# Performance work log

Hardware: AMD Instinct MI355X
Metric: run time of the kernel (lower is better)

## Reference

```python
import jax, jax.numpy as jnp
import numpy as np

HIDDEN = 1024
NUM_HEADS = 16
GROUP_SIZE = 2
GROUP_NUM = NUM_HEADS // GROUP_SIZE
HEAD_DIM = HIDDEN // NUM_HEADS


def setup_inputs() -> dict:
    key = jax.random.key(0)
    ks = jax.random.split(key, 9)
    B, S = 1, 4096
    s = 0.02
    return {
        "hidden_state": jax.random.normal(ks[0], (B, S, HIDDEN), jnp.float32),
        "Wq": jax.random.normal(ks[1], (HIDDEN, HIDDEN), jnp.float32) * s,
        "bq": jnp.zeros((HIDDEN,), jnp.float32),
        "Wk": jax.random.normal(ks[2], (HIDDEN, GROUP_NUM * HEAD_DIM), jnp.float32) * s,
        "bk": jnp.zeros((GROUP_NUM * HEAD_DIM,), jnp.float32),
        "Wv": jax.random.normal(ks[3], (HIDDEN, GROUP_NUM * HEAD_DIM), jnp.float32) * s,
        "bv": jnp.zeros((GROUP_NUM * HEAD_DIM,), jnp.float32),
        "Wo": jax.random.normal(ks[4], (HIDDEN, HIDDEN), jnp.float32) * s,
        "bo": jnp.zeros((HIDDEN,), jnp.float32),
    }


def reference(hidden_state, Wq, bq, Wk, bk, Wv, bv, Wo, bo):
    B, S, _ = hidden_state.shape
    # projections
    q = hidden_state @ Wq + bq                      # [B,S,H*hd]
    k = hidden_state @ Wk + bk                      # [B,S,G*hd]
    v = hidden_state @ Wv + bv                      # [B,S,G*hd]
    q = q.reshape(B, S, NUM_HEADS, HEAD_DIM).transpose(0, 2, 1, 3)   # [B,H,S,hd]
    k = k.reshape(B, S, GROUP_NUM, HEAD_DIM).transpose(0, 2, 1, 3)   # [B,G,S,hd]
    v = v.reshape(B, S, GROUP_NUM, HEAD_DIM).transpose(0, 2, 1, 3)
    # expand KV heads: each kv head repeated group_size times consecutively
    k = jnp.repeat(k, GROUP_SIZE, axis=1)           # [B,H,S,hd]
    v = jnp.repeat(v, GROUP_SIZE, axis=1)
    scale = 1.0 / np.sqrt(HEAD_DIM).astype(np.float32)
    scores = jnp.einsum('bhqd,bhkd->bhqk', q, k) * scale   # [B,H,S,S]
    attn = jax.nn.softmax(scores, axis=-1)
    ctx = jnp.einsum('bhqk,bhkd->bhqd', attn, v)    # [B,H,S,hd]
    ctx = ctx.transpose(0, 2, 1, 3).reshape(B, S, HIDDEN)
    return ctx @ Wo + bo
```

## Files before the change

### kernel.cpp

```cpp
#include <hip/hip_runtime.h>
#include <hip/hip_bf16.h>
#include <cstdint>
#include <cstddef>

typedef __bf16 bf16x8 __attribute__((ext_vector_type(8)));
typedef float f32x4 __attribute__((ext_vector_type(4)));
typedef float f32x16 __attribute__((ext_vector_type(16)));
typedef uint32_t u32x4 __attribute__((ext_vector_type(4)));
typedef __hip_bfloat16 bf16h;

__device__ __forceinline__ unsigned short bf16bits(float f) {
  bf16h h = __float2bfloat16(f);
  return __builtin_bit_cast(unsigned short, h);
}
__device__ __forceinline__ float bf16tof(unsigned short u) {
  union { uint32_t i; float f; } v; v.i = (uint32_t)u << 16; return v.f;
}

__global__ void cast_f32_bf16(const float* __restrict__ src, bf16h* __restrict__ dst, int n) {
  int i = (blockIdx.x * blockDim.x + threadIdx.x) * 4;
  if (i >= n) return;
  float4 v = *reinterpret_cast<const float4*>(src + i);
  ushort4 o;
  o.x = bf16bits(v.x); o.y = bf16bits(v.y); o.z = bf16bits(v.z); o.w = bf16bits(v.w);
  *reinterpret_cast<ushort4*>(dst + i) = o;
}

__global__ void transpose_cast_f32(const float* __restrict__ src, bf16h* __restrict__ dst,
                                   int R, int C, float scale) {
  __shared__ float tile[32][33];
  int c0 = blockIdx.x * 32, r0 = blockIdx.y * 32;
  int tx = threadIdx.x, ty = threadIdx.y;
  #pragma unroll
  for (int i = 0; i < 32; i += 8)
    tile[ty + i][tx] = src[(size_t)(r0 + ty + i) * C + c0 + tx];
  __syncthreads();
  #pragma unroll
  for (int i = 0; i < 32; i += 8)
    dst[(size_t)(c0 + ty + i) * R + r0 + tx] = __float2bfloat16(tile[tx][ty + i] * scale);
}

__global__ void concat_bias(const float* __restrict__ bq, const float* __restrict__ bk,
                            const float* __restrict__ bv, float* __restrict__ bcat, float qscale) {
  int i = blockIdx.x * blockDim.x + threadIdx.x;
  if (i >= 2048) return;
  bcat[i] = (i < 1024) ? bq[i] * qscale : (i < 1536 ? bk[i - 1024] : bv[i - 1536]);
}

__device__ __forceinline__ void store_out(float* p, float v) { *p = v; }
__device__ __forceinline__ void store_out(bf16h* p, float v) { *p = __float2bfloat16(v); }

template <typename OutT>
__global__ __launch_bounds__(256) void gemm_bt(const bf16h* __restrict__ A, const bf16h* __restrict__ BT,
                                               const float* __restrict__ bias, OutT* __restrict__ C,
                                               int ldc, bf16h* __restrict__ vtg, int vcol0,
                                               int M, int N, int K) {
  __shared__ __align__(16) bf16h As[128 * 64];
  __shared__ __align__(16) bf16h Bs[128 * 64];
  const int tid = threadIdx.x;
  const int lane = tid & 63;
  const int m0 = blockIdx.y * 128, n0 = blockIdx.x * 128;
  const int wid = tid >> 6, wr = wid >> 1, wc = wid & 1;
  const int cl = lane & 15, rg = lane >> 4;
  const int srow = tid >> 3, scol = (tid & 7) * 8;
  f32x4 acc[4][4] = {};

  for (int k0 = 0; k0 < K; k0 += 64) {
    __syncthreads();
    #pragma unroll
    for (int i = 0; i < 4; ++i) {
      int r = i * 32 + srow;
      __builtin_amdgcn_global_load_lds(
          (__attribute__((address_space(1))) void*)(A + (size_t)(m0 + r) * K + k0 + scol),
          (__attribute__((address_space(3))) void*)(As + i * 2048 + tid * 8), 16, 0, 0);
    }
    #pragma unroll
    for (int i = 0; i < 4; ++i) {
      int r = i * 32 + srow;
      __builtin_amdgcn_global_load_lds(
          (__attribute__((address_space(1))) void*)(BT + (size_t)(n0 + r) * K + k0 + scol),
          (__attribute__((address_space(3))) void*)(Bs + i * 2048 + tid * 8), 16, 0, 0);
    }
    __syncthreads();
    #pragma unroll
    for (int ks = 0; ks < 2; ++ks) {
      bf16x8 af[4], bfr[4];
      #pragma unroll
      for (int mi = 0; mi < 4; ++mi)
        af[mi] = *reinterpret_cast<const bf16x8*>(As + (wr * 64 + mi * 16 + cl) * 64 + ks * 32 + rg * 8);
      #pragma unroll
      for (int ni = 0; ni < 4; ++ni)
        bfr[ni] = *reinterpret_cast<const bf16x8*>(Bs + (wc * 64 + ni * 16 + cl) * 64 + ks * 32 + rg * 8);
      #pragma unroll
      for (int mi = 0; mi < 4; ++mi)
        #pragma unroll
        for (int ni = 0; ni < 4; ++ni)
          acc[mi][ni] = __builtin_amdgcn_mfma_f32_16x16x32_bf16(af[mi], bfr[ni], acc[mi][ni], 0, 0, 0);
    }
  }
  if (n0 >= vcol0) {
    #pragma unroll
    for (int ni = 0; ni < 4; ++ni) {
      int col = n0 + wc * 64 + ni * 16 + cl;
      float bv = bias[col];
      #pragma unroll
      for (int mi = 0; mi < 4; ++mi) {
        int row0 = m0 + wr * 64 + mi * 16 + rg * 4;
        ushort4 o;
        o.x = bf16bits(acc[mi][ni][0] + bv);
        o.y = bf16bits(acc[mi][ni][1] + bv);
        o.z = bf16bits(acc[mi][ni][2] + bv);
        o.w = bf16bits(acc[mi][ni][3] + bv);
        *reinterpret_cast<ushort4*>(vtg + (size_t)(col - vcol0) * 4096 + row0) = o;
      }
    }
  } else {
    #pragma unroll
    for (int ni = 0; ni < 4; ++ni) {
      int col = n0 + wc * 64 + ni * 16 + cl;
      float bv = bias[col];
      #pragma unroll
      for (int mi = 0; mi < 4; ++mi) {
        #pragma unroll
        for (int j = 0; j < 4; ++j) {
          int row = m0 + wr * 64 + mi * 16 + rg * 4 + j;
          store_out(&C[(size_t)row * ldc + col], acc[mi][ni][j] + bv);
        }
      }
    }
  }
}

__global__ __launch_bounds__(256, 2) void attn_fwd(const bf16h* __restrict__ qk,
                                                   const bf16h* __restrict__ vt,
                                                   bf16h* __restrict__ part,
                                                   float* __restrict__ lpart) {
  __shared__ __align__(16) char smem[32768];
  const int tid = threadIdx.x, lane = tid & 63, wid = tid >> 6;
  const int l31 = lane & 31, hi = lane >> 5;
  const int h = blockIdx.y, g = h >> 1, c = blockIdx.z;
  const int q0 = blockIdx.x * 256 + wid * 64;
  const int kbase = c * 2048;

  bf16x8 qfA[4], qfB[4];
  {
    const bf16h* qrowA = qk + (size_t)(q0 + l31) * 1536 + h * 64 + hi * 8;
    const bf16h* qrowB = qrowA + (size_t)32 * 1536;
    #pragma unroll
    for (int ds = 0; ds < 4; ++ds) {
      qfA[ds] = *reinterpret_cast<const bf16x8*>(qrowA + ds * 16);
      qfB[ds] = *reinterpret_cast<const bf16x8*>(qrowB + ds * 16);
    }
  }

  f32x16 oA0, oA1, oB0, oB1;
  #pragma unroll
  for (int i = 0; i < 16; ++i) { oA0[i] = 0.f; oA1[i] = 0.f; oB0[i] = 0.f; oB1[i] = 0.f; }
  float lsumA = 0.f, lsumB = 0.f;

  auto stage = [&](int kk, int b) {
    char* kb = smem + b * 16384;
    char* vb = kb + 8192;
    #pragma unroll
    for (int i = 0; i < 2; ++i) {
      int slot = tid + i * 256;
      int r = slot >> 3, s = slot & 7, sx = s ^ (r & 7);
      __builtin_amdgcn_global_load_lds(
          (__attribute__((address_space(1))) void*)(qk + (size_t)(kk + r) * 1536 + 1024 + g * 64 + sx * 8),
          (__attribute__((address_space(3))) void*)(kb + slot * 16), 16, 0, 0);
      __builtin_amdgcn_global_load_lds(
          (__attribute__((address_space(1))) void*)(vt + (size_t)(g * 64 + r) * 4096 + kk + sx * 8),
          (__attribute__((address_space(3))) void*)(vb + slot * 16), 16, 0, 0);
    }
  };

  stage(kbase, 0);
  __syncthreads();
  int cur = 0;

  auto build_pa = [&](const f32x16& S, int u) -> bf16x8 {
    uint32_t w0, w1, w2, w3;
    asm("v_cvt_pk_bf16_f32 %0, %1, %2" : "=v"(w0) : "v"(S[8 * u + 0]), "v"(S[8 * u + 1]));
    asm("v_cvt_pk_bf16_f32 %0, %1, %2" : "=v"(w1) : "v"(S[8 * u + 2]), "v"(S[8 * u + 3]));
    asm("v_cvt_pk_bf16_f32 %0, %1, %2" : "=v"(w2) : "v"(S[8 * u + 4]), "v"(S[8 * u + 5]));
    asm("v_cvt_pk_bf16_f32 %0, %1, %2" : "=v"(w3) : "v"(S[8 * u + 6]), "v"(S[8 * u + 7]));
    asm("v_permlane32_swap_b32 %0, %1" : "+v"(w0), "+v"(w2));
    asm("v_permlane32_swap_b32 %0, %1" : "+v"(w1), "+v"(w3));
    u32x4 pw; pw[0] = w0; pw[1] = w1; pw[2] = w2; pw[3] = w3;
    return __builtin_bit_cast(bf16x8, pw);
  };

  for (int tt = 0; tt < 32; ++tt) {
    if (tt < 31) stage(kbase + (tt + 1) * 64, cur ^ 1);
    const char* kb = smem + cur * 16384;
    const char* vb = kb + 8192;

    f32x16 sA0, sA1, sB0, sB1;
    #pragma unroll
    for (int i = 0; i < 16; ++i) { sA0[i] = 0.f; sA1[i] = 0.f; sB0[i] = 0.f; sB1[i] = 0.f; }
    __builtin_amdgcn_s_setprio(1);
    #pragma unroll
    for (int ds = 0; ds < 4; ++ds) {
      int cb = 32 * ds + 16 * hi;
      int r0 = l31, r1 = 32 + l31;
      bf16x8 k0 = *reinterpret_cast<const bf16x8*>(kb + ((r0 * 128 + cb) ^ ((r0 & 7) << 4)));
      bf16x8 k1 = *reinterpret_cast<const bf16x8*>(kb + ((r1 * 128 + cb) ^ ((r1 & 7) << 4)));
      sA0 = __builtin_amdgcn_mfma_f32_32x32x16_bf16(k0, qfA[ds], sA0, 0, 0, 0);
      sA1 = __builtin_amdgcn_mfma_f32_32x32x16_bf16(k1, qfA[ds], sA1, 0, 0, 0);
      sB0 = __builtin_amdgcn_mfma_f32_32x32x16_bf16(k0, qfB[ds], sB0, 0, 0, 0);
      sB1 = __builtin_amdgcn_mfma_f32_32x32x16_bf16(k1, qfB[ds], sB1, 0, 0, 0);
    }
    __builtin_amdgcn_s_setprio(0);

    float rsA = 0.f, rsB = 0.f;
    #pragma unroll
    for (int r = 0; r < 16; ++r) {
      sA0[r] = __builtin_amdgcn_exp2f(sA0[r]); rsA += sA0[r];
      sA1[r] = __builtin_amdgcn_exp2f(sA1[r]); rsA += sA1[r];
      sB0[r] = __builtin_amdgcn_exp2f(sB0[r]); rsB += sB0[r];
      sB1[r] = __builtin_amdgcn_exp2f(sB1[r]); rsB += sB1[r];
    }
    lsumA += rsA + __shfl_xor(rsA, 32);
    lsumB += rsB + __shfl_xor(rsB, 32);

    __builtin_amdgcn_s_setprio(1);
    #pragma unroll
    for (int ks = 0; ks < 4; ++ks) {
      const int u = ks & 1;
      bf16x8 paA = build_pa(ks < 2 ? sA0 : sA1, u);
      bf16x8 paB = build_pa(ks < 2 ? sB0 : sB1, u);
      int cb = 32 * ks + 16 * hi;
      int r0 = l31, r1 = 32 + l31;
      bf16x8 vf0 = *reinterpret_cast<const bf16x8*>(vb + ((r0 * 128 + cb) ^ ((r0 & 7) << 4)));
      bf16x8 vf1 = *reinterpret_cast<const bf16x8*>(vb + ((r1 * 128 + cb) ^ ((r1 & 7) << 4)));
      oA0 = __builtin_amdgcn_mfma_f32_32x32x16_bf16(vf0, paA, oA0, 0, 0, 0);
      oA1 = __builtin_amdgcn_mfma_f32_32x32x16_bf16(vf1, paA, oA1, 0, 0, 0);
      oB0 = __builtin_amdgcn_mfma_f32_32x32x16_bf16(vf0, paB, oB0, 0, 0, 0);
      oB1 = __builtin_amdgcn_mfma_f32_32x32x16_bf16(vf1, paB, oB1, 0, 0, 0);
    }
    __builtin_amdgcn_s_setprio(0);

    __syncthreads();
    cur ^= 1;
  }

  {
    int qA = q0 + l31, qB = qA + 32;
    bf16h* pA = part + ((size_t)(c * 4096 + qA) * 16 + h) * 64;
    bf16h* pB = part + ((size_t)(c * 4096 + qB) * 16 + h) * 64;
    #pragma unroll
    for (int dh = 0; dh < 2; ++dh) {
      const f32x16& aA = dh ? oA1 : oA0;
      const f32x16& aB = dh ? oB1 : oB0;
      #pragma unroll
      for (int t = 0; t < 4; ++t) {
        int d0 = dh * 32 + 8 * t + 4 * hi;
        ushort4 sa, sb;
        sa.x = bf16bits(aA[4 * t + 0]); sa.y = bf16bits(aA[4 * t + 1]);
        sa.z = bf16bits(aA[4 * t + 2]); sa.w = bf16bits(aA[4 * t + 3]);
        sb.x = bf16bits(aB[4 * t + 0]); sb.y = bf16bits(aB[4 * t + 1]);
        sb.z = bf16bits(aB[4 * t + 2]); sb.w = bf16bits(aB[4 * t + 3]);
        *reinterpret_cast<ushort4*>(pA + d0) = sa;
        *reinterpret_cast<ushort4*>(pB + d0) = sb;
      }
    }
    if (hi == 0) {
      lpart[(size_t)(c * 4096 + qA) * 16 + h] = lsumA;
      lpart[(size_t)(c * 4096 + qB) * 16 + h] = lsumB;
    }
  }
}

__global__ __launch_bounds__(256) void combine_part(const bf16h* __restrict__ part,
                                                    const float* __restrict__ lpart,
                                                    bf16h* __restrict__ ctx) {
  int idx = blockIdx.x * 256 + threadIdx.x;
  int q = idx >> 4, h = idx & 15;
  const bf16h* p0 = part + ((size_t)q * 16 + h) * 64;
  const bf16h* p1 = p0 + (size_t)4096 * 1024;
  float inv = 1.0f / (lpart[(size_t)q * 16 + h] + lpart[(size_t)4096 * 16 + q * 16 + h]);
  bf16h* o = ctx + (size_t)q * 1024 + h * 64;
  #pragma unroll
  for (int w = 0; w < 8; ++w) {
    ushort4 a = *reinterpret_cast<const ushort4*>(p0 + w * 8);
    ushort4 b = *reinterpret_cast<const ushort4*>(p1 + w * 8);
    ushort4 c2 = *reinterpret_cast<const ushort4*>(p0 + w * 8 + 4);
    ushort4 d2 = *reinterpret_cast<const ushort4*>(p1 + w * 8 + 4);
    ushort4 r0, r1;
    r0.x = bf16bits((bf16tof(a.x) + bf16tof(b.x)) * inv);
    r0.y = bf16bits((bf16tof(a.y) + bf16tof(b.y)) * inv);
    r0.z = bf16bits((bf16tof(a.z) + bf16tof(b.z)) * inv);
    r0.w = bf16bits((bf16tof(a.w) + bf16tof(b.w)) * inv);
    r1.x = bf16bits((bf16tof(c2.x) + bf16tof(d2.x)) * inv);
    r1.y = bf16bits((bf16tof(c2.y) + bf16tof(d2.y)) * inv);
    r1.z = bf16bits((bf16tof(c2.z) + bf16tof(d2.z)) * inv);
    r1.w = bf16bits((bf16tof(c2.w) + bf16tof(d2.w)) * inv);
    *reinterpret_cast<ushort4*>(o + w * 8) = r0;
    *reinterpret_cast<ushort4*>(o + w * 8 + 4) = r1;
  }
}

extern "C" void kernel_launch(void* const* d_in, const int* in_sizes, int n_in,
                              void* d_out, int out_size, void* d_ws, size_t ws_size,
                              hipStream_t stream) {
  const float* hs = (const float*)d_in[0];
  const float* Wq = (const float*)d_in[1];
  const float* bq = (const float*)d_in[2];
  const float* Wk = (const float*)d_in[3];
  const float* bk = (const float*)d_in[4];
  const float* Wv = (const float*)d_in[5];
  const float* bv = (const float*)d_in[6];
  const float* Wo = (const float*)d_in[7];
  const float* bo = (const float*)d_in[8];
  float* out = (float*)d_out;

  const float QSCALE = 0.125f * 1.44269504088896f;

  char* ws = (char*)d_ws;
  const size_t MB = 1u << 20;
  bf16h* hb    = (bf16h*)(ws);
  bf16h* WcT   = (bf16h*)(ws + 8 * MB);
  bf16h* part  = (bf16h*)(ws);
  float* lpart = (float*)(ws + 16 * MB);
  bf16h* qk    = (bf16h*)(ws + 17 * MB);
  bf16h* ctx   = (bf16h*)(ws + 17 * MB);
  bf16h* vtg   = (bf16h*)(ws + 29 * MB);
  bf16h* WoT   = (bf16h*)(ws + 33 * MB);
  float* bcat  = (float*)(ws + 35 * MB);

  cast_f32_bf16<<<dim3(4096), dim3(256), 0, stream>>>(hs, hb, 4096 * 1024);
  transpose_cast_f32<<<dim3(32, 32), dim3(32, 8), 0, stream>>>(Wq, WcT, 1024, 1024, QSCALE);
  transpose_cast_f32<<<dim3(16, 32), dim3(32, 8), 0, stream>>>(Wk, WcT + 1024 * 1024, 1024, 512, 1.0f);
  transpose_cast_f32<<<dim3(16, 32), dim3(32, 8), 0, stream>>>(Wv, WcT + 1536 * 1024, 1024, 512, 1.0f);
  transpose_cast_f32<<<dim3(32, 32), dim3(32, 8), 0, stream>>>(Wo, WoT, 1024, 1024, 1.0f);
  concat_bias<<<dim3(8), dim3(256), 0, stream>>>(bq, bk, bv, bcat, QSCALE);
  gemm_bt<bf16h><<<dim3(16, 32), dim3(256), 0, stream>>>(hb, WcT, bcat, qk, 1536, vtg, 1536,
                                                         4096, 2048, 1024);
  attn_fwd<<<dim3(16, 16, 2), dim3(256), 0, stream>>>(qk, vtg, part, lpart);
  combine_part<<<dim3(256), dim3(256), 0, stream>>>(part, lpart, ctx);
  gemm_bt<float><<<dim3(8, 32), dim3(256), 0, stream>>>(ctx, WoT, bo, out, 1024, (bf16h*)nullptr,
                                                        0x40000000, 4096, 1024, 1024);
}
```

Before: 158.5 us.

## Load K/V fragments directly from global memory, dropping LDS staging and barriers

The attention kernel no longer stages K and V tiles into shared memory with double-buffered global_load_lds and per-iteration __syncthreads. Each wave now reads its K and V MFMA fragments straight from global memory, relying on L2/L1 caching to serve the reuse across the four waves of a block. The V loads are issued early so they overlap the exp2 pass, and the row-sum reduction is split into several independent accumulators to shorten its dependency chain. This removes barrier stalls and LDS traffic but loses the explicit prefetch, so every wave redundantly fetches the same K/V data and global load latency sits directly in the loop.

```diff
diff --git a/kernel.cpp b/kernel.cpp
--- a/kernel.cpp
+++ b/kernel.cpp
@@ -135,7 +135,6 @@
                                                    const bf16h* __restrict__ vt,
                                                    bf16h* __restrict__ part,
                                                    float* __restrict__ lpart) {
-  __shared__ __align__(16) char smem[32768];
   const int tid = threadIdx.x, lane = tid & 63, wid = tid >> 6;
   const int l31 = lane & 31, hi = lane >> 5;
   const int h = blockIdx.y, g = h >> 1, c = blockIdx.z;
@@ -153,30 +152,13 @@
     }
   }
 
+  const bf16h* kp = qk + (size_t)(kbase + l31) * 1536 + 1024 + g * 64 + 8 * hi;
+  const bf16h* vp = vt + (size_t)(g * 64 + l31) * 4096 + kbase + 8 * hi;
+
   f32x16 oA0, oA1, oB0, oB1;
   #pragma unroll
   for (int i = 0; i < 16; ++i) { oA0[i] = 0.f; oA1[i] = 0.f; oB0[i] = 0.f; oB1[i] = 0.f; }
   float lsumA = 0.f, lsumB = 0.f;
-
-  auto stage = [&](int kk, int b) {
-    char* kb = smem + b * 16384;
-    char* vb = kb + 8192;
-    #pragma unroll
-    for (int i = 0; i < 2; ++i) {
-      int slot = tid + i * 256;
-      int r = slot >> 3, s = slot & 7, sx = s ^ (r & 7);
-      __builtin_amdgcn_global_load_lds(
-          (__attribute__((address_space(1))) void*)(qk + (size_t)(kk + r) * 1536 + 1024 + g * 64 + sx * 8),
-          (__attribute__((address_space(3))) void*)(kb + slot * 16), 16, 0, 0);
-      __builtin_amdgcn_global_load_lds(
-          (__attribute__((address_space(1))) void*)(vt + (size_t)(g * 64 + r) * 4096 + kk + sx * 8),
-          (__attribute__((address_space(3))) void*)(vb + slot * 16), 16, 0, 0);
-    }
-  };
-
-  stage(kbase, 0);
-  __syncthreads();
-  int cur = 0;
 
   auto build_pa = [&](const f32x16& S, int u) -> bf16x8 {
     uint32_t w0, w1, w2, w3;
@@ -191,9 +173,8 @@
   };
 
   for (int tt = 0; tt < 32; ++tt) {
-    if (tt < 31) stage(kbase + (tt + 1) * 64, cur ^ 1);
-    const char* kb = smem + cur * 16384;
-    const char* vb = kb + 8192;
+    const bf16h* kt = kp + (size_t)(tt * 64) * 1536;
+    const bf16h* vtp = vp + tt * 64;
 
     f32x16 sA0, sA1, sB0, sB1;
     #pragma unroll
@@ -201,10 +182,8 @@
     __builtin_amdgcn_s_setprio(1);
     #pragma unroll
     for (int ds = 0; ds < 4; ++ds) {
-      int cb = 32 * ds + 16 * hi;
-      int r0 = l31, r1 = 32 + l31;
-      bf16x8 k0 = *reinterpret_cast<const bf16x8*>(kb + ((r0 * 128 + cb) ^ ((r0 & 7) << 4)));
-      bf16x8 k1 = *reinterpret_cast<const bf16x8*>(kb + ((r1 * 128 + cb) ^ ((r1 & 7) << 4)));
+      bf16x8 k0 = *reinterpret_cast<const bf16x8*>(kt + 16 * ds);
+      bf16x8 k1 = *reinterpret_cast<const bf16x8*>(kt + (size_t)32 * 1536 + 16 * ds);
       sA0 = __builtin_amdgcn_mfma_f32_32x32x16_bf16(k0, qfA[ds], sA0, 0, 0, 0);
       sA1 = __builtin_amdgcn_mfma_f32_32x32x16_bf16(k1, qfA[ds], sA1, 0, 0, 0);
       sB0 = __builtin_amdgcn_mfma_f32_32x32x16_bf16(k0, qfB[ds], sB0, 0, 0, 0);
@@ -212,14 +191,31 @@
     }
     __builtin_amdgcn_s_setprio(0);
 
-    float rsA = 0.f, rsB = 0.f;
-    #pragma unroll
-    for (int r = 0; r < 16; ++r) {
-      sA0[r] = __builtin_amdgcn_exp2f(sA0[r]); rsA += sA0[r];
-      sA1[r] = __builtin_amdgcn_exp2f(sA1[r]); rsA += sA1[r];
-      sB0[r] = __builtin_amdgcn_exp2f(sB0[r]); rsB += sB0[r];
-      sB1[r] = __builtin_amdgcn_exp2f(sB1[r]); rsB += sB1[r];
-    }
+    bf16x8 vf[4][2];
+    #pragma unroll
+    for (int ks = 0; ks < 4; ++ks) {
+      vf[ks][0] = *reinterpret_cast<const bf16x8*>(vtp + 16 * ks);
+      vf[ks][1] = *reinterpret_cast<const bf16x8*>(vtp + (size_t)32 * 4096 + 16 * ks);
+    }
+
+    float ra0 = 0.f, ra1 = 0.f, ra2 = 0.f, ra3 = 0.f;
+    float rb0 = 0.f, rb1 = 0.f, rb2 = 0.f, rb3 = 0.f;
+    #pragma unroll
+    for (int r = 0; r < 16; r += 4) {
+      #pragma unroll
+      for (int j = 0; j < 4; ++j) {
+        sA0[r + j] = __builtin_amdgcn_exp2f(sA0[r + j]);
+        sA1[r + j] = __builtin_amdgcn_exp2f(sA1[r + j]);
+        sB0[r + j] = __builtin_amdgcn_exp2f(sB0[r + j]);
+        sB1[r + j] = __builtin_amdgcn_exp2f(sB1[r + j]);
+      }
+      ra0 += sA0[r] + sA0[r + 1]; ra1 += sA0[r + 2] + sA0[r + 3];
+      ra2 += sA1[r] + sA1[r + 1]; ra3 += sA1[r + 2] + sA1[r + 3];
+      rb0 += sB0[r] + sB0[r + 1]; rb1 += sB0[r + 2] + sB0[r + 3];
+      rb2 += sB1[r] + sB1[r + 1]; rb3 += sB1[r + 2] + sB1[r + 3];
+    }
+    float rsA = (ra0 + ra1) + (ra2 + ra3);
+    float rsB = (rb0 + rb1) + (rb2 + rb3);
     lsumA += rsA + __shfl_xor(rsA, 32);
     lsumB += rsB + __shfl_xor(rsB, 32);
 
@@ -229,19 +225,12 @@
       const int u = ks & 1;
       bf16x8 paA = build_pa(ks < 2 ? sA0 : sA1, u);
       bf16x8 paB = build_pa(ks < 2 ? sB0 : sB1, u);
-      int cb = 32 * ks + 16 * hi;
-      int r0 = l31, r1 = 32 + l31;
-      bf16x8 vf0 = *reinterpret_cast<const bf16x8*>(vb + ((r0 * 128 + cb) ^ ((r0 & 7) << 4)));
-      bf16x8 vf1 = *reinterpret_cast<const bf16x8*>(vb + ((r1 * 128 + cb) ^ ((r1 & 7) << 4)));
-      oA0 = __builtin_amdgcn_mfma_f32_32x32x16_bf16(vf0, paA, oA0, 0, 0, 0);
-      oA1 = __builtin_amdgcn_mfma_f32_32x32x16_bf16(vf1, paA, oA1, 0, 0, 0);
-      oB0 = __builtin_amdgcn_mfma_f32_32x32x16_bf16(vf0, paB, oB0, 0, 0, 0);
-      oB1 = __builtin_amdgcn_mfma_f32_32x32x16_bf16(vf1, paB, oB1, 0, 0, 0);
+      oA0 = __builtin_amdgcn_mfma_f32_32x32x16_bf16(vf[ks][0], paA, oA0, 0, 0, 0);
+      oA1 = __builtin_amdgcn_mfma_f32_32x32x16_bf16(vf[ks][1], paA, oA1, 0, 0, 0);
+      oB0 = __builtin_amdgcn_mfma_f32_32x32x16_bf16(vf[ks][0], paB, oB0, 0, 0, 0);
+      oB1 = __builtin_amdgcn_mfma_f32_32x32x16_bf16(vf[ks][1], paB, oB1, 0, 0, 0);
     }
     __builtin_amdgcn_s_setprio(0);
-
-    __syncthreads();
-    cur ^= 1;
   }
 
   {
```

Result: slower. 209.8 us (+32.4%).

## Deepen attention K/V pipeline to 4 LDS buffers with vmcnt waits

Applied to the files above, without the earlier changes.

The attention loop goes from double buffering to a 4-slot ring in LDS, prefetching two tiles ahead. The per-iteration __syncthreads after compute is replaced by an explicit s_waitcnt vmcnt plus a single s_barrier at the top of the loop. Separately, the exp2 row-sum reduction is split into several independent accumulators to shorten the dependency chain. LDS grows to 64KB per block, which may lower occupancy below the launch-bounds target of 2 blocks per CU. The hand-set vmcnt counts depend on how many loads stage() issues.

```diff
diff --git a/kernel.cpp b/kernel.cpp
--- a/kernel.cpp
+++ b/kernel.cpp
@@ -8,6 +8,8 @@
 typedef float f32x16 __attribute__((ext_vector_type(16)));
 typedef uint32_t u32x4 __attribute__((ext_vector_type(4)));
 typedef __hip_bfloat16 bf16h;
+
+#define WAITVM(N) asm volatile("s_waitcnt vmcnt(" #N ")" ::: "memory")
 
 __device__ __forceinline__ unsigned short bf16bits(float f) {
   bf16h h = __float2bfloat16(f);
@@ -135,7 +137,7 @@
                                                    const bf16h* __restrict__ vt,
                                                    bf16h* __restrict__ part,
                                                    float* __restrict__ lpart) {
-  __shared__ __align__(16) char smem[32768];
+  __shared__ __align__(16) char smem[4 * 16384];
   const int tid = threadIdx.x, lane = tid & 63, wid = tid >> 6;
   const int l31 = lane & 31, hi = lane >> 5;
   const int h = blockIdx.y, g = h >> 1, c = blockIdx.z;
@@ -173,10 +175,6 @@
           (__attribute__((address_space(3))) void*)(vb + slot * 16), 16, 0, 0);
     }
   };
-
-  stage(kbase, 0);
-  __syncthreads();
-  int cur = 0;
 
   auto build_pa = [&](const f32x16& S, int u) -> bf16x8 {
     uint32_t w0, w1, w2, w3;
@@ -190,9 +188,18 @@
     return __builtin_bit_cast(bf16x8, pw);
   };
 
+  stage(kbase, 0);
+  stage(kbase + 64, 1);
+
   for (int tt = 0; tt < 32; ++tt) {
-    if (tt < 31) stage(kbase + (tt + 1) * 64, cur ^ 1);
-    const char* kb = smem + cur * 16384;
+    if (tt + 2 < 32) stage(kbase + (tt + 2) * 64, (tt + 2) & 3);
+    if (tt < 30)      WAITVM(8);
+    else if (tt == 30) WAITVM(4);
+    else               WAITVM(0);
+    __builtin_amdgcn_s_barrier();
+    __builtin_amdgcn_sched_barrier(0);
+
+    const char* kb = smem + (tt & 3) * 16384;
     const char* vb = kb + 8192;
 
     f32x16 sA0, sA1, sB0, sB1;
@@ -212,14 +219,24 @@
     }
     __builtin_amdgcn_s_setprio(0);
 
-    float rsA = 0.f, rsB = 0.f;
-    #pragma unroll
-    for (int r = 0; r < 16; ++r) {
-      sA0[r] = __builtin_amdgcn_exp2f(sA0[r]); rsA += sA0[r];
-      sA1[r] = __builtin_amdgcn_exp2f(sA1[r]); rsA += sA1[r];
-      sB0[r] = __builtin_amdgcn_exp2f(sB0[r]); rsB += sB0[r];
-      sB1[r] = __builtin_amdgcn_exp2f(sB1[r]); rsB += sB1[r];
-    }
+    float ra0 = 0.f, ra1 = 0.f, ra2 = 0.f, ra3 = 0.f;
+    float rb0 = 0.f, rb1 = 0.f, rb2 = 0.f, rb3 = 0.f;
+    #pragma unroll
+    for (int r = 0; r < 16; r += 4) {
+      #pragma unroll
+      for (int j = 0; j < 4; ++j) {
+        sA0[r + j] = __builtin_amdgcn_exp2f(sA0[r + j]);
+        sA1[r + j] = __builtin_amdgcn_exp2f(sA1[r + j]);
+        sB0[r + j] = __builtin_amdgcn_exp2f(sB0[r + j]);
+        sB1[r + j] = __builtin_amdgcn_exp2f(sB1[r + j]);
+      }
+      ra0 += sA0[r] + sA0[r + 1]; ra1 += sA0[r + 2] + sA0[r + 3];
+      ra2 += sA1[r] + sA1[r + 1]; ra3 += sA1[r + 2] + sA1[r + 3];
+      rb0 += sB0[r] + sB0[r + 1]; rb1 += sB0[r + 2] + sB0[r + 3];
+      rb2 += sB1[r] + sB1[r + 1]; rb3 += sB1[r + 2] + sB1[r + 3];
+    }
+    float rsA = (ra0 + ra1) + (ra2 + ra3);
+    float rsB = (rb0 + rb1) + (rb2 + rb3);
     lsumA += rsA + __shfl_xor(rsA, 32);
     lsumB += rsB + __shfl_xor(rsB, 32);
 
@@ -239,9 +256,7 @@
       oB1 = __builtin_amdgcn_mfma_f32_32x32x16_bf16(vf1, paB, oB1, 0, 0, 0);
     }
     __builtin_amdgcn_s_setprio(0);
-
-    __syncthreads();
-    cur ^= 1;
+    __builtin_amdgcn_sched_barrier(0);
   }
 
   {
```

Result: no change. 160.0 us (+0.9%).
